# Kernel optimization log

Measured on AMD Instinct MI355X. Metric: run time of the kernel, lower is better.

## Reference

```python
import jax, jax.numpy as jnp
import numpy as np

B, L, D, H = 8, 256, 256, 8
DH = D // H
NEG = jnp.float32(-(2 ** 32) + 1)


def _split_heads(x):
    # [B, L, D] -> [H, B, L, DH]  (tf.split axis=2 + concat axis=0 stacks heads slowest)
    b, l, d = x.shape
    return x.reshape(b, l, H, DH).transpose(2, 0, 1, 3)


def _split_heads_t(t):
    # [B, L, L, D] -> [H, B, L, L, DH]
    b, q, k, d = t.shape
    return t.reshape(b, q, k, H, DH).transpose(3, 0, 1, 2, 4)


def setup_inputs() -> dict:
    key = jax.random.key(0)
    ks = jax.random.split(key, 12)
    s = 1.0 / np.sqrt(D)
    return {
        "queries": jax.random.normal(ks[0], (B, L, D), jnp.float32),
        "keys": jax.random.normal(ks[1], (B, L, D), jnp.float32),
        "time_matrix_K": jax.random.normal(ks[2], (B, L, L, D), jnp.float32),
        "time_matrix_V": jax.random.normal(ks[3], (B, L, L, D), jnp.float32),
        "absolute_pos_K": jax.random.normal(ks[4], (B, L, D), jnp.float32),
        "absolute_pos_V": jax.random.normal(ks[5], (B, L, D), jnp.float32),
        "Wq": jax.random.normal(ks[6], (D, D), jnp.float32) * s,
        "bq": jnp.zeros((D,), jnp.float32),
        "Wk": jax.random.normal(ks[7], (D, D), jnp.float32) * s,
        "bk": jnp.zeros((D,), jnp.float32),
        "Wv": jax.random.normal(ks[8], (D, D), jnp.float32) * s,
        "bv": jnp.zeros((D,), jnp.float32),
    }


def reference(queries, keys, time_matrix_K, time_matrix_V,
              absolute_pos_K, absolute_pos_V, Wq, bq, Wk, bk, Wv, bv):
    Qh = _split_heads(queries @ Wq + bq)          # [H,B,L,DH]
    Kh = _split_heads(keys @ Wk + bk)
    Vh = _split_heads(keys @ Wv + bv)
    Pk = _split_heads(absolute_pos_K)
    Pv = _split_heads(absolute_pos_V)
    Tk = _split_heads_t(time_matrix_K)            # [H,B,L,L,DH]
    Tv = _split_heads_t(time_matrix_V)

    scores = (jnp.einsum('hbqd,hbkd->hbqk', Qh, Kh)
              + jnp.einsum('hbqd,hbkd->hbqk', Qh, Pk)
              + jnp.einsum('hbqkd,hbqd->hbqk', Tk, Qh))
    scores = scores / jnp.float32(np.sqrt(DH))

    # key padding mask: rows of `keys` summing to exactly 0 are padding
    key_mask = jnp.sign(jnp.abs(jnp.sum(keys, axis=-1)))   # [B,L]
    scores = jnp.where(key_mask[None, :, None, :] == 0, NEG, scores)
    # causal mask
    tril = jnp.tril(jnp.ones((L, L), jnp.float32))
    scores = jnp.where(tril[None, None, :, :] == 0, NEG, scores)

    attn = jax.nn.softmax(scores, axis=-1)                  # [H,B,L,L]
    query_mask = jnp.sign(jnp.abs(jnp.sum(queries, axis=-1)))  # [B,L]
    attn = attn * query_mask[None, :, :, None]
    # dropout is identity at inference (dropout_rate=0)

    out = (jnp.einsum('hbqk,hbkd->hbqd', attn, Vh)
           + jnp.einsum('hbqk,hbkd->hbqd', attn, Pv)
           + jnp.einsum('hbqk,hbqkd->hbqd', attn, Tv))      # [H,B,L,DH]

    out = out.transpose(1, 2, 0, 3).reshape(B, L, D)        # concat heads
    return out + queries
```

## Files before the change

### kernel.cpp

```cpp
#include <hip/hip_runtime.h>

#define L 256
#define D 256
#define H 8
#define DH 32

static constexpr float NEGV = -4294967296.0f;
static constexpr float INV_SQRT_DH = 0.17677669529663687f;

__global__ __launch_bounds__(256) void proj3_kernel(
    const float* __restrict__ queries, const float* __restrict__ keys,
    const float* __restrict__ Wq, const float* __restrict__ bq,
    const float* __restrict__ Wk, const float* __restrict__ bk,
    const float* __restrict__ Wv, const float* __restrict__ bv,
    const float* __restrict__ pk, const float* __restrict__ pv,
    float* __restrict__ Qo, float* __restrict__ KPko, float* __restrict__ VPvo)
{
    __shared__ float As[16][68];
    __shared__ float Bs[16][64];

    const float* A; const float* W; const float* bias; const float* add; float* out;
    if (blockIdx.z == 0)      { A = queries; W = Wq; bias = bq; add = nullptr; out = Qo; }
    else if (blockIdx.z == 1) { A = keys;    W = Wk; bias = bk; add = pk;      out = KPko; }
    else                      { A = keys;    W = Wv; bias = bv; add = pv;      out = VPvo; }

    const int t  = threadIdx.x;
    const int bm = blockIdx.x * 64;
    const int bn = blockIdx.y * 64;

    const int ar = t >> 2;
    const int ak = (t & 3) << 2;
    const int br = t >> 4;
    const int bc = (t & 15) << 2;
    const int tm = (t >> 4) << 2;
    const int tn = (t & 15) << 2;

    float acc[4][4] = {};

    for (int k0 = 0; k0 < 256; k0 += 16) {
        const float4 a4 = *(const float4*)&A[(bm + ar) * 256 + k0 + ak];
        const float4 b4 = *(const float4*)&W[(k0 + br) * 256 + bn + bc];
        As[ak + 0][ar] = a4.x; As[ak + 1][ar] = a4.y;
        As[ak + 2][ar] = a4.z; As[ak + 3][ar] = a4.w;
        *(float4*)&Bs[br][bc] = b4;
        __syncthreads();

        #pragma unroll
        for (int kk = 0; kk < 16; ++kk) {
            const float4 a = *(const float4*)&As[kk][tm];
            const float4 bb = *(const float4*)&Bs[kk][tn];
            const float aa[4] = {a.x, a.y, a.z, a.w};
            const float bbv[4] = {bb.x, bb.y, bb.z, bb.w};
            #pragma unroll
            for (int i = 0; i < 4; ++i)
                #pragma unroll
                for (int jj = 0; jj < 4; ++jj)
                    acc[i][jj] = fmaf(aa[i], bbv[jj], acc[i][jj]);
        }
        __syncthreads();
    }

    const float4 bias4 = *(const float4*)&bias[bn + tn];
    #pragma unroll
    for (int i = 0; i < 4; ++i) {
        const int row = bm + tm + i;
        float4 o;
        o.x = acc[i][0] + bias4.x; o.y = acc[i][1] + bias4.y;
        o.z = acc[i][2] + bias4.z; o.w = acc[i][3] + bias4.w;
        if (add) {
            const float4 a4 = *(const float4*)&add[row * 256 + bn + tn];
            o.x += a4.x; o.y += a4.y; o.z += a4.z; o.w += a4.w;
        }
        *(float4*)&out[row * 256 + bn + tn] = o;
    }
}

__global__ __launch_bounds__(256) void mask_kernel(
    const float* __restrict__ keys, const float* __restrict__ queries,
    float* __restrict__ kmask, float* __restrict__ qmask)
{
    const int wid  = (blockIdx.x * 256 + threadIdx.x) >> 6;
    const int lane = threadIdx.x & 63;
    const float* src = (wid < 2048) ? keys : queries;
    const int row = (wid < 2048) ? wid : (wid - 2048);

    const float4 v = *(const float4*)&src[row * 256 + (lane << 2)];
    float s = v.x + v.y + v.z + v.w;
    #pragma unroll
    for (int o = 1; o < 64; o <<= 1) s += __shfl_xor(s, o);
    if (lane == 0) {
        const float m = (s != 0.0f) ? 1.0f : 0.0f;
        if (wid < 2048) kmask[row] = m; else qmask[row] = m;
    }
}

__global__ __launch_bounds__(256) void attn_fused_kernel(
    const float* __restrict__ Qm, const float* __restrict__ KPk,
    const float* __restrict__ VPv, const float* __restrict__ Tk,
    const float* __restrict__ Tv, const float* __restrict__ kmask,
    const float* __restrict__ qmask, const float* __restrict__ queries,
    float* __restrict__ out)
{
    const int bid = blockIdx.x;
    const int b   = bid >> 8;
    const int j0  = bid & 255;
    const int q   = (b & 1) ? (255 - j0) : j0;
    const int bq  = (b << 8) + q;
    const int t    = threadIdx.x;
    const int w    = t >> 6;
    const int lane = t & 63;

    __shared__ float  kmrow[L];
    __shared__ float4 accL[4][64];
    __shared__ float  mL[4][64];
    __shared__ float  lL[4][64];

    kmrow[t] = kmask[(b << 8) + t];
    __syncthreads();

    const size_t tbase = (size_t)bq << 16;
    const float4 qv = *(const float4*)&Qm[bq * 256 + (lane << 2)];

    float  m  = NEGV;
    float  ls = 0.0f;
    float4 acc = make_float4(0.f, 0.f, 0.f, 0.f);

    #pragma unroll 2
    for (int k = w; k <= q; k += 4) {
        const float4 kv  = *(const float4*)&KPk[((b << 8) + k) * 256 + (lane << 2)];
        const float4 tkv = *(const float4*)&Tk[tbase + ((size_t)k << 8) + (lane << 2)];
        const float4 vv  = *(const float4*)&VPv[((b << 8) + k) * 256 + (lane << 2)];
        const float4 tvv = *(const float4*)&Tv[tbase + ((size_t)k << 8) + (lane << 2)];

        float p = qv.x * (kv.x + tkv.x);
        p = fmaf(qv.y, kv.y + tkv.y, p);
        p = fmaf(qv.z, kv.z + tkv.z, p);
        p = fmaf(qv.w, kv.w + tkv.w, p);
        p += __shfl_xor(p, 1);
        p += __shfl_xor(p, 2);
        p += __shfl_xor(p, 4);

        const float s = (kmrow[k] != 0.0f) ? p * INV_SQRT_DH : NEGV;
        const float mn = fmaxf(m, s);
        const float f  = __expf(m - mn);
        const float e  = __expf(s - mn);
        ls = fmaf(ls, f, e);
        acc.x = fmaf(e, vv.x + tvv.x, acc.x * f);
        acc.y = fmaf(e, vv.y + tvv.y, acc.y * f);
        acc.z = fmaf(e, vv.z + tvv.z, acc.z * f);
        acc.w = fmaf(e, vv.w + tvv.w, acc.w * f);
        m = mn;
    }

    accL[w][lane] = acc;
    mL[w][lane]   = m;
    lL[w][lane]   = ls;
    __syncthreads();

    if (t < 64) {
        const float m0 = mL[0][t], m1 = mL[1][t], m2 = mL[2][t], m3 = mL[3][t];
        const float M  = fmaxf(fmaxf(m0, m1), fmaxf(m2, m3));
        float li = 0.0f;
        float4 o = make_float4(0.f, 0.f, 0.f, 0.f);
        #pragma unroll
        for (int i = 0; i < 4; ++i) {
            const float f = __expf(mL[i][t] - M);
            li = fmaf(lL[i][t], f, li);
            const float4 a4 = accL[i][t];
            o.x = fmaf(a4.x, f, o.x);
            o.y = fmaf(a4.y, f, o.y);
            o.z = fmaf(a4.z, f, o.z);
            o.w = fmaf(a4.w, f, o.w);
        }
        if (M == NEGV) {
            for (int k = q + 1; k < L; ++k) {
                const float4 vv  = *(const float4*)&VPv[((b << 8) + k) * 256 + (t << 2)];
                const float4 tvv = *(const float4*)&Tv[tbase + ((size_t)k << 8) + (t << 2)];
                o.x += vv.x + tvv.x;
                o.y += vv.y + tvv.y;
                o.z += vv.z + tvv.z;
                o.w += vv.w + tvv.w;
            }
            li = 256.0f;
        }
        const float r   = 1.0f / li;
        const float qmv = qmask[bq];
        const float4 qv2 = *(const float4*)&queries[bq * 256 + (t << 2)];
        float4 ov;
        ov.x = o.x * r * qmv + qv2.x;
        ov.y = o.y * r * qmv + qv2.y;
        ov.z = o.z * r * qmv + qv2.z;
        ov.w = o.w * r * qmv + qv2.w;
        *(float4*)&out[bq * 256 + (t << 2)] = ov;
    }
}

extern "C" void kernel_launch(void* const* d_in, const int* in_sizes, int n_in,
                              void* d_out, int out_size, void* d_ws, size_t ws_size,
                              hipStream_t stream)
{
    const float* queries = (const float*)d_in[0];
    const float* keys    = (const float*)d_in[1];
    const float* Tk      = (const float*)d_in[2];
    const float* Tv      = (const float*)d_in[3];
    const float* pk      = (const float*)d_in[4];
    const float* pv      = (const float*)d_in[5];
    const float* Wq      = (const float*)d_in[6];
    const float* bq      = (const float*)d_in[7];
    const float* Wk      = (const float*)d_in[8];
    const float* bk      = (const float*)d_in[9];
    const float* Wv      = (const float*)d_in[10];
    const float* bv      = (const float*)d_in[11];
    float* out = (float*)d_out;

    float* ws  = (float*)d_ws;
    float* Q   = ws;
    float* KPk = ws + 524288;
    float* VPv = ws + 1048576;
    float* km  = ws + 1572864;
    float* qm  = ws + 1574912;

    dim3 pgrid(2048 / 64, 256 / 64, 3);
    proj3_kernel<<<pgrid, 256, 0, stream>>>(queries, keys, Wq, bq, Wk, bk,
                                            Wv, bv, pk, pv, Q, KPk, VPv);
    mask_kernel<<<1024, 256, 0, stream>>>(keys, queries, km, qm);
    attn_fused_kernel<<<2048, 256, 0, stream>>>(Q, KPk, VPv, Tk, Tv, km, qm,
                                                queries, out);
}
```

Measured before the change: 148.5 us.

## Split causal key range into halves across paired queries with separate combine kernel

Each attention block now handles two queries (q and 255-q), processing half of each query's causal key range, so every block does roughly equal work instead of varying with q. Partial softmax state (max, sum, accumulator) per half is written to workspace and merged by a new combine kernel that also applies the fully-masked fallback, query mask and residual. This targets the load imbalance of causal attention, at the cost of an extra kernel launch and a round trip through global memory for the partials.

```diff
diff --git a/kernel.cpp b/kernel.cpp
--- a/kernel.cpp
+++ b/kernel.cpp
@@ -94,18 +94,15 @@
     }
 }
 
-__global__ __launch_bounds__(256) void attn_fused_kernel(
+__global__ __launch_bounds__(256) void attn_part_kernel(
     const float* __restrict__ Qm, const float* __restrict__ KPk,
     const float* __restrict__ VPv, const float* __restrict__ Tk,
     const float* __restrict__ Tv, const float* __restrict__ kmask,
-    const float* __restrict__ qmask, const float* __restrict__ queries,
-    float* __restrict__ out)
+    float* __restrict__ pm, float* __restrict__ pl, float4* __restrict__ pacc)
 {
     const int bid = blockIdx.x;
     const int b   = bid >> 8;
-    const int j0  = bid & 255;
-    const int q   = (b & 1) ? (255 - j0) : j0;
-    const int bq  = (b << 8) + q;
+    const int jj  = bid & 255;
     const int t    = threadIdx.x;
     const int w    = t >> 6;
     const int lane = t & 63;
@@ -118,81 +115,128 @@
     kmrow[t] = kmask[(b << 8) + t];
     __syncthreads();
 
-    const size_t tbase = (size_t)bq << 16;
-    const float4 qv = *(const float4*)&Qm[bq * 256 + (lane << 2)];
-
-    float  m  = NEGV;
-    float  ls = 0.0f;
-    float4 acc = make_float4(0.f, 0.f, 0.f, 0.f);
-
-    #pragma unroll 2
-    for (int k = w; k <= q; k += 4) {
-        const float4 kv  = *(const float4*)&KPk[((b << 8) + k) * 256 + (lane << 2)];
-        const float4 tkv = *(const float4*)&Tk[tbase + ((size_t)k << 8) + (lane << 2)];
-        const float4 vv  = *(const float4*)&VPv[((b << 8) + k) * 256 + (lane << 2)];
-        const float4 tvv = *(const float4*)&Tv[tbase + ((size_t)k << 8) + (lane << 2)];
-
-        float p = qv.x * (kv.x + tkv.x);
-        p = fmaf(qv.y, kv.y + tkv.y, p);
-        p = fmaf(qv.z, kv.z + tkv.z, p);
-        p = fmaf(qv.w, kv.w + tkv.w, p);
-        p += __shfl_xor(p, 1);
-        p += __shfl_xor(p, 2);
-        p += __shfl_xor(p, 4);
-
-        const float s = (kmrow[k] != 0.0f) ? p * INV_SQRT_DH : NEGV;
-        const float mn = fmaxf(m, s);
-        const float f  = __expf(m - mn);
-        const float e  = __expf(s - mn);
-        ls = fmaf(ls, f, e);
-        acc.x = fmaf(e, vv.x + tvv.x, acc.x * f);
-        acc.y = fmaf(e, vv.y + tvv.y, acc.y * f);
-        acc.z = fmaf(e, vv.z + tvv.z, acc.z * f);
-        acc.w = fmaf(e, vv.w + tvv.w, acc.w * f);
-        m = mn;
-    }
-
-    accL[w][lane] = acc;
-    mL[w][lane]   = m;
-    lL[w][lane]   = ls;
-    __syncthreads();
-
-    if (t < 64) {
-        const float m0 = mL[0][t], m1 = mL[1][t], m2 = mL[2][t], m3 = mL[3][t];
-        const float M  = fmaxf(fmaxf(m0, m1), fmaxf(m2, m3));
-        float li = 0.0f;
-        float4 o = make_float4(0.f, 0.f, 0.f, 0.f);
-        #pragma unroll
-        for (int i = 0; i < 4; ++i) {
-            const float f = __expf(mL[i][t] - M);
-            li = fmaf(lL[i][t], f, li);
-            const float4 a4 = accL[i][t];
-            o.x = fmaf(a4.x, f, o.x);
-            o.y = fmaf(a4.y, f, o.y);
-            o.z = fmaf(a4.z, f, o.z);
-            o.w = fmaf(a4.w, f, o.w);
-        }
-        if (M == NEGV) {
-            for (int k = q + 1; k < L; ++k) {
-                const float4 vv  = *(const float4*)&VPv[((b << 8) + k) * 256 + (t << 2)];
-                const float4 tvv = *(const float4*)&Tv[tbase + ((size_t)k << 8) + (t << 2)];
-                o.x += vv.x + tvv.x;
-                o.y += vv.y + tvv.y;
-                o.z += vv.z + tvv.z;
-                o.w += vv.w + tvv.w;
+    #pragma unroll
+    for (int half = 0; half < 2; ++half) {
+        const int q   = half ? (255 - jj) : jj;
+        const int bq  = (b << 8) + q;
+        const int s   = (q + 2) >> 1;
+        const int klo = half ? s : 0;
+        const int khi = half ? (q + 1) : s;
+        const size_t tbase = (size_t)bq << 16;
+        const float4 qv = *(const float4*)&Qm[bq * 256 + (lane << 2)];
+
+        float  m  = NEGV;
+        float  ls = 0.0f;
+        float4 acc = make_float4(0.f, 0.f, 0.f, 0.f);
+
+        #pragma unroll 2
+        for (int k = klo + w; k < khi; k += 4) {
+            const float4 kv  = *(const float4*)&KPk[((b << 8) + k) * 256 + (lane << 2)];
+            const float4 tkv = *(const float4*)&Tk[tbase + ((size_t)k << 8) + (lane << 2)];
+            const float4 vv  = *(const float4*)&VPv[((b << 8) + k) * 256 + (lane << 2)];
+            const float4 tvv = *(const float4*)&Tv[tbase + ((size_t)k << 8) + (lane << 2)];
+
+            float p = qv.x * (kv.x + tkv.x);
+            p = fmaf(qv.y, kv.y + tkv.y, p);
+            p = fmaf(qv.z, kv.z + tkv.z, p);
+            p = fmaf(qv.w, kv.w + tkv.w, p);
+            p += __shfl_xor(p, 1);
+            p += __shfl_xor(p, 2);
+            p += __shfl_xor(p, 4);
+
+            const float sv = (kmrow[k] != 0.0f) ? p * INV_SQRT_DH : NEGV;
+            const float mn = fmaxf(m, sv);
+            const float f  = __expf(m - mn);
+            const float e  = __expf(sv - mn);
+            ls = fmaf(ls, f, e);
+            acc.x = fmaf(e, vv.x + tvv.x, acc.x * f);
+            acc.y = fmaf(e, vv.y + tvv.y, acc.y * f);
+            acc.z = fmaf(e, vv.z + tvv.z, acc.z * f);
+            acc.w = fmaf(e, vv.w + tvv.w, acc.w * f);
+            m = mn;
+        }
+
+        accL[w][lane] = acc;
+        mL[w][lane]   = m;
+        lL[w][lane]   = ls;
+        __syncthreads();
+
+        if (t < 64) {
+            const float m0 = mL[0][t], m1 = mL[1][t], m2 = mL[2][t], m3 = mL[3][t];
+            const float M  = fmaxf(fmaxf(m0, m1), fmaxf(m2, m3));
+            float li = 0.0f;
+            float4 o = make_float4(0.f, 0.f, 0.f, 0.f);
+            #pragma unroll
+            for (int i = 0; i < 4; ++i) {
+                const float f = __expf(mL[i][t] - M);
+                li = fmaf(lL[i][t], f, li);
+                const float4 a4 = accL[i][t];
+                o.x = fmaf(a4.x, f, o.x);
+                o.y = fmaf(a4.y, f, o.y);
+                o.z = fmaf(a4.z, f, o.z);
+                o.w = fmaf(a4.w, f, o.w);
             }
-            li = 256.0f;
-        }
-        const float r   = 1.0f / li;
-        const float qmv = qmask[bq];
-        const float4 qv2 = *(const float4*)&queries[bq * 256 + (t << 2)];
-        float4 ov;
-        ov.x = o.x * r * qmv + qv2.x;
-        ov.y = o.y * r * qmv + qv2.y;
-        ov.z = o.z * r * qmv + qv2.z;
-        ov.w = o.w * r * qmv + qv2.w;
-        *(float4*)&out[bq * 256 + (t << 2)] = ov;
-    }
+            const int idx = ((bq << 1) + half) << 6;
+            pm[idx + t]   = M;
+            pl[idx + t]   = li;
+            pacc[idx + t] = o;
+        }
+        __syncthreads();
+    }
+}
+
+__global__ __launch_bounds__(64) void attn_comb_kernel(
+    const float* __restrict__ pm, const float* __restrict__ pl,
+    const float4* __restrict__ pacc, const float* __restrict__ VPv,
+    const float* __restrict__ Tv, const float* __restrict__ qmask,
+    const float* __restrict__ queries, float* __restrict__ out)
+{
+    const int bq = blockIdx.x;
+    const int b  = bq >> 8;
+    const int q  = bq & 255;
+    const int t  = threadIdx.x;
+
+    const int i0 = ((bq << 1) + 0) << 6;
+    const int i1 = ((bq << 1) + 1) << 6;
+    const float  m0 = pm[i0 + t], m1 = pm[i1 + t];
+    const float  l0 = pl[i0 + t], l1 = pl[i1 + t];
+    const float4 a0 = pacc[i0 + t], a1 = pacc[i1 + t];
+    const float  M  = fmaxf(m0, m1);
+
+    float li;
+    float4 o;
+    if (M == NEGV) {
+        o.x = a0.x + a1.x; o.y = a0.y + a1.y;
+        o.z = a0.z + a1.z; o.w = a0.w + a1.w;
+        const size_t tbase = (size_t)bq << 16;
+        for (int k = q + 1; k < L; ++k) {
+            const float4 vv  = *(const float4*)&VPv[((b << 8) + k) * 256 + (t << 2)];
+            const float4 tvv = *(const float4*)&Tv[tbase + ((size_t)k << 8) + (t << 2)];
+            o.x += vv.x + tvv.x;
+            o.y += vv.y + tvv.y;
+            o.z += vv.z + tvv.z;
+            o.w += vv.w + tvv.w;
+        }
+        li = 256.0f;
+    } else {
+        const float f0 = __expf(m0 - M);
+        const float f1 = __expf(m1 - M);
+        li = fmaf(l0, f0, l1 * f1);
+        o.x = fmaf(a0.x, f0, a1.x * f1);
+        o.y = fmaf(a0.y, f0, a1.y * f1);
+        o.z = fmaf(a0.z, f0, a1.z * f1);
+        o.w = fmaf(a0.w, f0, a1.w * f1);
+    }
+
+    const float r   = 1.0f / li;
+    const float qmv = qmask[bq];
+    const float4 qv = *(const float4*)&queries[bq * 256 + (t << 2)];
+    float4 ov;
+    ov.x = o.x * r * qmv + qv.x;
+    ov.y = o.y * r * qmv + qv.y;
+    ov.z = o.z * r * qmv + qv.z;
+    ov.w = o.w * r * qmv + qv.w;
+    *(float4*)&out[bq * 256 + (t << 2)] = ov;
 }
 
 extern "C" void kernel_launch(void* const* d_in, const int* in_sizes, int n_in,
@@ -213,17 +257,22 @@
     const float* bv      = (const float*)d_in[11];
     float* out = (float*)d_out;
 
-    float* ws  = (float*)d_ws;
-    float* Q   = ws;
-    float* KPk = ws + 524288;
-    float* VPv = ws + 1048576;
-    float* km  = ws + 1572864;
-    float* qm  = ws + 1574912;
+    float*  ws   = (float*)d_ws;
+    float*  Q    = ws;
+    float*  KPk  = ws + 524288;
+    float*  VPv  = ws + 1048576;
+    float*  km   = ws + 1572864;
+    float*  qm   = ws + 1574912;
+    float*  pm   = ws + 1576960;
+    float*  pl   = ws + 1839104;
+    float4* pacc = (float4*)(ws + 2101248);
 
     dim3 pgrid(2048 / 64, 256 / 64, 3);
     proj3_kernel<<<pgrid, 256, 0, stream>>>(queries, keys, Wq, bq, Wk, bk,
                                             Wv, bv, pk, pv, Q, KPk, VPv);
     mask_kernel<<<1024, 256, 0, stream>>>(keys, queries, km, qm);
-    attn_fused_kernel<<<2048, 256, 0, stream>>>(Q, KPk, VPv, Tk, Tv, km, qm,
-                                                queries, out);
-}
+    attn_part_kernel<<<2048, 256, 0, stream>>>(Q, KPk, VPv, Tk, Tv, km,
+                                               pm, pl, pacc);
+    attn_comb_kernel<<<2048, 64, 0, stream>>>(pm, pl, pacc, VPv, Tv, qm,
+                                              queries, out);
+}
```

New measurement: 155.6 us. 1.05x slower.
